# Kernel tuning notes

Hardware: AMD Instinct MI355X
Metric: run time of the kernel (lower is better)

Reference implementation:

```python
import jax, jax.numpy as jnp
import numpy as np

K = 3          # kernel size
STRIDE = 1
PAD = 1
DIL = 1
K2 = K * K


def setup_inputs() -> dict:
    key = jax.random.key(0)
    ks = jax.random.split(key, 5)
    B, Cin, Cout, H, W = 8, 128, 128, 64, 64
    x = jax.random.normal(ks[0], (B, Cin, H, W), jnp.float32)
    # conv_offset_mask: Conv2d(Cin, 3*dg*K*K=27, 3x3). Original inits to zero;
    # use small random weights so offsets are nonzero sub-pixel shifts.
    w_off = jax.random.normal(ks[1], (3 * K2, Cin, K, K), jnp.float32) * 0.05
    b_off = jax.random.normal(ks[2], (3 * K2,), jnp.float32) * 0.1
    weight = jax.random.normal(ks[3], (Cout, Cin, K, K), jnp.float32) / np.sqrt(Cin * K2)
    bias = jax.random.normal(ks[4], (Cout,), jnp.float32) * 0.1
    return dict(x=x, w_off=w_off, b_off=b_off, weight=weight, bias=bias)


def _conv(x, w, b):
    y = jax.lax.conv_general_dilated(
        x, w, (STRIDE, STRIDE), [(PAD, PAD), (PAD, PAD)],
        dimension_numbers=('NCHW', 'OIHW', 'NCHW'))
    return y + b[None, :, None, None]


def _sample_one(xb, pyb, pxb, mb):
    Cin, Hin, Win = xb.shape
    y0 = jnp.floor(pyb)
    x0 = jnp.floor(pxb)
    wy = pyb - y0   # fractional weights
    wx = pxb - x0
    y0i = y0.astype(jnp.int32)
    x0i = x0.astype(jnp.int32)
    xf = xb.reshape(Cin, -1)

    def g(yi, xi):
        valid = ((yi >= 0) & (yi < Hin) & (xi >= 0) & (xi < Win)).astype(xb.dtype)
        idx = jnp.clip(yi, 0, Hin - 1) * Win + jnp.clip(xi, 0, Win - 1)
        return xf[:, idx] * valid[None]   # [Cin,K2,Ho,Wo]

    v = (g(y0i, x0i) * ((1 - wy) * (1 - wx))[None]
         + g(y0i, x0i + 1) * ((1 - wy) * wx)[None]
         + g(y0i + 1, x0i) * (wy * (1 - wx))[None]
         + g(y0i + 1, x0i + 1) * (wy * wx)[None])
    return v * mb[None]   # modulated columns [Cin,K2,Ho,Wo]


def reference(x, w_off, b_off, weight, bias):
    B, Cin, Hin, Win = x.shape
    Cout = weight.shape[0]
    om = _conv(x, w_off, b_off)                 # [B, 3*K2, Ho, Wo]
    dy = om[:, :K2]
    dx = om[:, K2:2 * K2]
    m = jax.nn.sigmoid(om[:, 2 * K2:])          # modulation mask
    Ho, Wo = dy.shape[2], dy.shape[3]
    kh = jnp.repeat(jnp.arange(K), K)           # [K2] kernel row per tap
    kw = jnp.tile(jnp.arange(K), K)             # [K2] kernel col per tap
    grid_y = jnp.arange(Ho) * STRIDE - PAD
    grid_x = jnp.arange(Wo) * STRIDE - PAD
    py = dy + grid_y[None, None, :, None] + (kh * DIL)[None, :, None, None]
    px = dx + grid_x[None, None, None, :] + (kw * DIL)[None, :, None, None]
    cols = jax.vmap(_sample_one)(x, py, px, m)  # [B,Cin,K2,Ho,Wo]
    out = jnp.einsum('bckhw,ock->bohw', cols, weight.reshape(Cout, Cin, K2))
    return out + bias[None, :, None, None]
```

## Files before the change

### kernel.cpp

```cpp
#include <hip/hip_runtime.h>
#include <math.h>

#define BATCH 8
#define CIN   128
#define COUT  128
#define HH    64
#define WW    64
#define OC    27
#define KDIM  1152

typedef unsigned short u16;
typedef unsigned int   u32;
typedef __attribute__((ext_vector_type(8))) short bf16x8;
typedef __attribute__((ext_vector_type(4))) float f32x4;

__device__ __forceinline__ float b2f(u16 u) {
    return __uint_as_float((u32)u << 16);
}
__device__ __forceinline__ u16 f2b(float f) {
    u32 u = __float_as_uint(f);
    return (u16)((u + 0x7fffu + ((u >> 16) & 1u)) >> 16);
}
__device__ __forceinline__ float blo(u32 u) { return __uint_as_float(u << 16); }
__device__ __forceinline__ float bhi(u32 u) { return __uint_as_float(u & 0xffff0000u); }
__device__ __forceinline__ u32 cvtpk(float lo, float hi) {
    u32 r;
    asm("v_cvt_pk_bf16_f32 %0, %1, %2" : "=v"(r) : "v"(lo), "v"(hi));
    return r;
}
__device__ __forceinline__ bf16x8 pack8(u32 a, u32 b, u32 c, u32 d) {
    union { u32 u[4]; bf16x8 v; } z;
    z.u[0] = a; z.u[1] = b; z.u[2] = c; z.u[3] = d;
    return z.v;
}

__device__ __forceinline__ int xswiz(int o, int K) { return (o & 7) * K + (o >> 3); }

__global__ __launch_bounds__(256) void k_prep(const float* __restrict__ x,
                                              const float* __restrict__ weight,
                                              const float* __restrict__ w_off,
                                              u16* __restrict__ xtb,
                                              u16* __restrict__ wbf,
                                              u16* __restrict__ wop) {
    __shared__ float tile[64][65];
    int gbid = blockIdx.x;
    int t = threadIdx.x;
    if (gbid < 1024) {
        int bid = xswiz(gbid, 128);
        int b   = bid >> 7;
        int c0  = ((bid >> 6) & 1) << 6;
        int hw0 = (bid & 63) << 6;
        int ln  = t & 63;
        int cq  = t >> 6;
#pragma unroll
        for (int r = 0; r < 16; ++r) {
            int c_l = cq * 16 + r;
            tile[c_l][ln] = x[(((size_t)(b * CIN + c0 + c_l)) << 12) + hw0 + ln];
        }
        __syncthreads();
#pragma unroll
        for (int r = 0; r < 16; ++r) {
            int hw_w = cq * 16 + r;
            xtb[((size_t)(b << 12) + hw0 + hw_w) * 128 + c0 + ln] = f2b(tile[ln][hw_w]);
        }
    } else if (gbid < 1600) {
        int tid = (gbid - 1024) * 256 + t;
        int j  = tid & 7;
        int l  = (tid >> 3) & 63;
        int ni = (tid >> 9) & 7;
        int s  = (tid >> 12) & 3;
        int t9 = tid >> 14;
        int co = ni * 16 + (l & 15);
        int ci = s * 32 + ((l >> 4) << 3) + j;
        wbf[tid] = f2b(weight[co * KDIM + ci * 9 + t9]);
    } else {
        int tid = (gbid - 1600) * 256 + t;
        int j   = tid & 7;
        int l   = (tid >> 3) & 63;
        int ni  = (tid >> 9) & 1;
        int sg  = (tid >> 10) & 3;
        int rest = tid >> 12;
        int t9  = rest % 9;
        int split = rest / 9;
        int co = ni * 16 + (l & 15);
        int ci = sg * 32 + ((l >> 4) << 3) + j;
        float val = (co < OC) ? w_off[co * KDIM + ci * 9 + t9] : 0.f;
        u16 hi = f2b(val);
        u16 lo = f2b(val - b2f(hi));
        wop[tid] = split ? lo : hi;
    }
}

#define CST 228
__global__ __launch_bounds__(512, 4) void k_fused(const float* __restrict__ x,
                                                  const u16* __restrict__ xtb,
                                                  const u16* __restrict__ wop,
                                                  const u16* __restrict__ wbf,
                                                  const float* __restrict__ b_off,
                                                  const float* __restrict__ bias,
                                                  float* __restrict__ out) {
    __shared__ __align__(16) char smem[73472];
    float* Xf  = (float*)smem;
    float* red = (float*)(smem + 58368);
    float* omf = (float*)(smem + 66560);

    const int t  = threadIdx.x;
    const int lb = xswiz(blockIdx.x, 64);
    const int b  = lb >> 6;
    const int h  = lb & 63;
    const int l    = t & 63;
    const int wv   = t >> 6;
    const int l15  = l & 15;
    const int lg   = l >> 4;

    {
        const int ntile = wv & 3;
        const int kgrp  = wv >> 2;

        if (t < 192) {
            int ci = t & 63, row = t >> 6;
            int idx = ci * CST + row * 68 + (((ci >> 3) & 3) << 3) + 64;
            *(float4*)(Xf + idx) = make_float4(0.f, 0.f, 0.f, 0.f);
        }

        f32x4 acc0 = {0.f, 0.f, 0.f, 0.f};
        f32x4 acc1 = {0.f, 0.f, 0.f, 0.f};
        float4 st_[6];

        auto stageA_load = [&](int half) {
#pragma unroll
            for (int it = 0; it < 6; ++it) {
                int slot = t + it * 512;
                int pair = slot >> 4, ln16 = slot & 15;
                int row = pair >> 6, ci = pair & 63;
                int grow = h - 1 + row;
                float4 v = make_float4(0.f, 0.f, 0.f, 0.f);
                if ((unsigned)grow < 64u)
                    v = *(const float4*)(x + (((size_t)(b * CIN + half * 64 + ci)) << 12)
                                           + (grow << 6) + ln16 * 4);
                st_[it] = v;
            }
        };
        auto stageA_store = [&]() {
#pragma unroll
            for (int it = 0; it < 6; ++it) {
                int slot = t + it * 512;
                int pair = slot >> 4, ln16 = slot & 15;
                int row = pair >> 6, ci = pair & 63;
                int idx = ci * CST + row * 68 + (((ci >> 3) & 3) << 3) + ln16 * 4;
                *(float4*)(Xf + idx) = st_[it];
            }
        };
        auto kloopA = [&](int half) {
            for (int tap = 0; tap < 9; ++tap) {
                int kh = tap / 3, kw = tap - kh * 3;
                int gw = ntile * 16 + kw - 1 + l15;
                int px = (gw < 0) ? 64 : ((gw > 63) ? 65 : gw);
                int ci0 = kgrp * 32 + (lg << 3);
                int base = ci0 * CST + kh * 68 + (((ci0 >> 3) & 3) << 3) + px;
                float f0 = Xf[base], f1 = Xf[base + CST];
                float f2 = Xf[base + 2 * CST], f3 = Xf[base + 3 * CST];
                float f4 = Xf[base + 4 * CST], f5 = Xf[base + 5 * CST];
                float f6 = Xf[base + 6 * CST], f7 = Xf[base + 7 * CST];
                u32 h0 = cvtpk(f0, f1), h1 = cvtpk(f2, f3);
                u32 h2 = cvtpk(f4, f5), h3 = cvtpk(f6, f7);
                u32 l0 = cvtpk(f0 - blo(h0), f1 - bhi(h0));
                u32 l1 = cvtpk(f2 - blo(h1), f3 - bhi(h1));
                u32 l2 = cvtpk(f4 - blo(h2), f5 - bhi(h2));
                u32 l3 = cvtpk(f6 - blo(h3), f7 - bhi(h3));
                bf16x8 ah = pack8(h0, h1, h2, h3);
                bf16x8 al = pack8(l0, l1, l2, l3);
                int sg = half * 2 + kgrp;
                const u16* B = wop + (((tap * 4 + sg) * 2) << 9) + (l << 3);
                bf16x8 wh0 = *(const bf16x8*)(B);
                bf16x8 wh1 = *(const bf16x8*)(B + 512);
                bf16x8 wl0 = *(const bf16x8*)(B + 36864);
                bf16x8 wl1 = *(const bf16x8*)(B + 36864 + 512);
                acc0 = __builtin_amdgcn_mfma_f32_16x16x32_bf16(wh0, ah, acc0, 0, 0, 0);
                acc1 = __builtin_amdgcn_mfma_f32_16x16x32_bf16(wh1, ah, acc1, 0, 0, 0);
                acc0 = __builtin_amdgcn_mfma_f32_16x16x32_bf16(wl0, ah, acc0, 0, 0, 0);
                acc1 = __builtin_amdgcn_mfma_f32_16x16x32_bf16(wl1, ah, acc1, 0, 0, 0);
                acc0 = __builtin_amdgcn_mfma_f32_16x16x32_bf16(wh0, al, acc0, 0, 0, 0);
                acc1 = __builtin_amdgcn_mfma_f32_16x16x32_bf16(wh1, al, acc1, 0, 0, 0);
            }
        };

        stageA_load(0);
        stageA_store();
        __syncthreads();
        stageA_load(1);
        kloopA(0);
        __syncthreads();
        stageA_store();
        __syncthreads();
        kloopA(1);

        if (kgrp) {
            float* rp = red + (((ntile << 6) + l) << 3);
            *(f32x4*)rp = acc0;
            *(f32x4*)(rp + 4) = acc1;
        }
        __syncthreads();
        if (!kgrp) {
            const float* rp = red + (((ntile << 6) + l) << 3);
            acc0 += *(const f32x4*)rp;
            acc1 += *(const f32x4*)(rp + 4);
            int px = ntile * 16 + l15;
            int co0 = lg << 2;
#pragma unroll
            for (int r = 0; r < 4; ++r)
                omf[((co0 + r) << 6) + px] = acc0[r] + b_off[co0 + r];
            int co1 = 16 + (lg << 2);
#pragma unroll
            for (int r = 0; r < 4; ++r) {
                int co = co1 + r;
                if (co < OC) {
                    float v = acc1[r] + b_off[co];
                    if (co >= 18) v = 1.f / (1.f + expf(-v));
                    omf[(co << 6) + px] = v;
                }
            }
        }
        __syncthreads();
    }

    float (*w4)[4] = (float (*)[4])(smem + 32768);
    int* y0c = (int*)(smem + 41984);
    int* x0c = (int*)(smem + 44288);
    int* y1c = (int*)(smem + 46592);
    int* x1c = (int*)(smem + 48896);

    for (int i = t; i < 576; i += 512) {
        int p  = i / 9;
        int tt = i - p * 9;
        float dy = omf[(tt << 6) + p];
        float dx = omf[((9 + tt) << 6) + p];
        float m  = omf[((18 + tt) << 6) + p];
        float py = dy + (float)(h - 1 + tt / 3);
        float px = dx + (float)(p - 1 + tt % 3);
        float y0f = floorf(py), x0f = floorf(px);
        float wy = py - y0f, wx = px - x0f;
        int y0 = (int)y0f, x0 = (int)x0f;
        int y1 = y0 + 1,   x1 = x0 + 1;
        float vy0 = ((unsigned)y0 < 64u) ? 1.f : 0.f;
        float vy1 = ((unsigned)y1 < 64u) ? 1.f : 0.f;
        float vx0 = ((unsigned)x0 < 64u) ? 1.f : 0.f;
        float vx1 = ((unsigned)x1 < 64u) ? 1.f : 0.f;
        w4[i][0] = (1.f - wy) * (1.f - wx) * m * vy0 * vx0;
        w4[i][1] = (1.f - wy) * wx         * m * vy0 * vx1;
        w4[i][2] = wy         * (1.f - wx) * m * vy1 * vx0;
        w4[i][3] = wy         * wx         * m * vy1 * vx1;
        y0c[i] = min(max(y0, 0), 63);
        y1c[i] = min(max(y1, 0), 63);
        x0c[i] = min(max(x0, 0), 63);
        x1c[i] = min(max(x1, 0), 63);
    }
    __syncthreads();

    f32x4 acc[4][2];
#pragma unroll
    for (int pt = 0; pt < 4; ++pt)
#pragma unroll
        for (int nt = 0; nt < 2; ++nt) acc[pt][nt] = (f32x4){0.f, 0.f, 0.f, 0.f};

    const int grp  = t >> 8;
    const int tl   = t & 255;
    const int l2   = tl & 63;
    const int wv2  = tl >> 6;
    const int row0 = l2 & 15;
    const int kg   = l2 >> 4;

    const int sp = tl >> 2;
    const int sc = tl & 3;
    const u16* xb = xtb + ((size_t)b << 19);

    uint4 g_[2][4];

    auto sample_load = [&](int tt) {
        int pi = sp * 9 + tt;
        int o00 = (((y0c[pi] << 6) | x0c[pi]) << 7) + grp * 64;
        int o01 = (((y0c[pi] << 6) | x1c[pi]) << 7) + grp * 64;
        int o10 = (((y1c[pi] << 6) | x0c[pi]) << 7) + grp * 64;
        int o11 = (((y1c[pi] << 6) | x1c[pi]) << 7) + grp * 64;
#pragma unroll
        for (int k = 0; k < 2; ++k) {
            int ch = k * 32 + sc * 8;
            g_[k][0] = *(const uint4*)(xb + o00 + ch);
            g_[k][1] = *(const uint4*)(xb + o01 + ch);
            g_[k][2] = *(const uint4*)(xb + o10 + ch);
            g_[k][3] = *(const uint4*)(xb + o11 + ch);
        }
    };

    auto sample_finish = [&](int tt, int buf) {
        int pi = sp * 9 + tt;
        float4 W = *(const float4*)(&w4[pi][0]);
        u16* dst = (u16*)(smem + buf * 16384);
#pragma unroll
        for (int k = 0; k < 2; ++k) {
            uint4 a00 = g_[k][0], a01 = g_[k][1], a10 = g_[k][2], a11 = g_[k][3];
            uint4 ow;
            {
                float e0 = W.x * blo(a00.x) + W.y * blo(a01.x) + W.z * blo(a10.x) + W.w * blo(a11.x);
                float e1 = W.x * bhi(a00.x) + W.y * bhi(a01.x) + W.z * bhi(a10.x) + W.w * bhi(a11.x);
                ow.x = cvtpk(e0, e1);
            }
            {
                float e0 = W.x * blo(a00.y) + W.y * blo(a01.y) + W.z * blo(a10.y) + W.w * blo(a11.y);
                float e1 = W.x * bhi(a00.y) + W.y * bhi(a01.y) + W.z * bhi(a10.y) + W.w * bhi(a11.y);
                ow.y = cvtpk(e0, e1);
            }
            {
                float e0 = W.x * blo(a00.z) + W.y * blo(a01.z) + W.z * blo(a10.z) + W.w * blo(a11.z);
                float e1 = W.x * bhi(a00.z) + W.y * bhi(a01.z) + W.z * bhi(a10.z) + W.w * bhi(a11.z);
                ow.z = cvtpk(e0, e1);
            }
            {
                float e0 = W.x * blo(a00.w) + W.y * blo(a01.w) + W.z * blo(a10.w) + W.w * blo(a11.w);
                float e1 = W.x * bhi(a00.w) + W.y * bhi(a01.w) + W.z * bhi(a10.w) + W.w * bhi(a11.w);
                ow.w = cvtpk(e0, e1);
            }
            int q16 = (grp * 8 + k * 4 + sc) ^ (sp & 15);
            *(uint4*)((char*)dst + (sp << 8) + (q16 << 4)) = ow;
        }
    };

    auto domfma = [&](int t9, int buf) {
        const char* Ab = (const char*)(smem + buf * 16384);
#pragma unroll
        for (int shalf = 0; shalf < 2; ++shalf) {
            int s = grp * 2 + shalf;
            int q = s * 4 + kg;
            int sw = (q ^ row0) << 4;
            bf16x8 a[4];
#pragma unroll
            for (int pt = 0; pt < 4; ++pt)
                a[pt] = *(const bf16x8*)(Ab + ((pt * 16 + row0) << 8) + sw);
            const u16* B = wbf + ((size_t)t9 << 14) + (s << 12) + (wv2 << 10) + (l2 << 3);
            bf16x8 b0 = *(const bf16x8*)(B);
            bf16x8 b1 = *(const bf16x8*)(B + 512);
#pragma unroll
            for (int pt = 0; pt < 4; ++pt) {
                acc[pt][0] = __builtin_amdgcn_mfma_f32_16x16x32_bf16(a[pt], b0, acc[pt][0], 0, 0, 0);
                acc[pt][1] = __builtin_amdgcn_mfma_f32_16x16x32_bf16(a[pt], b1, acc[pt][1], 0, 0, 0);
            }
        }
    };

    sample_load(0);
    sample_finish(0, 0);
    __syncthreads();
    for (int tt = 0; tt < 9; ++tt) {
        if (tt < 8) sample_load(tt + 1);
        domfma(tt, tt & 1);
        if (tt < 8) sample_finish(tt + 1, (tt + 1) & 1);
        __syncthreads();
    }

    float* outs = (float*)smem;
    if (grp) {
#pragma unroll
        for (int pt = 0; pt < 4; ++pt)
#pragma unroll
            for (int nt = 0; nt < 2; ++nt) {
                int co  = wv2 * 32 + nt * 16 + row0;
                int pxq = pt * 4 + kg;
                *(f32x4*)((char*)outs + (co << 8) + ((pxq ^ (co & 7)) << 4)) = acc[pt][nt];
            }
    }
    __syncthreads();
    if (!grp) {
#pragma unroll
        for (int pt = 0; pt < 4; ++pt)
#pragma unroll
            for (int nt = 0; nt < 2; ++nt) {
                int co  = wv2 * 32 + nt * 16 + row0;
                int pxq = pt * 4 + kg;
                char* ad = (char*)outs + (co << 8) + ((pxq ^ (co & 7)) << 4);
                f32x4 v = *(const f32x4*)ad;
                *(f32x4*)ad = v + acc[pt][nt];
            }
    }
    __syncthreads();
    {
        int co = t >> 2, qt = t & 3;
        float bb = bias[co];
        float* og = out + (((size_t)(b * COUT + co)) << 12) + (h << 6);
#pragma unroll
        for (int j = 0; j < 4; ++j) {
            int pxq = qt * 4 + j;
            f32x4 v = *(const f32x4*)((const char*)outs + (co << 8) + ((pxq ^ (co & 7)) << 4));
            float4 r = make_float4(v.x + bb, v.y + bb, v.z + bb, v.w + bb);
            *reinterpret_cast<float4*>(og + pxq * 4) = r;
        }
    }
}

extern "C" void kernel_launch(void* const* d_in, const int* in_sizes, int n_in,
                              void* d_out, int out_size, void* d_ws, size_t ws_size,
                              hipStream_t stream) {
    const float* x      = (const float*)d_in[0];
    const float* w_off  = (const float*)d_in[1];
    const float* b_off  = (const float*)d_in[2];
    const float* weight = (const float*)d_in[3];
    const float* bias   = (const float*)d_in[4];
    float* out = (float*)d_out;

    u16* xtb = (u16*)d_ws;
    u16* wbf = xtb + 4194304;
    u16* wop = wbf + 147456;

    k_prep<<<1888, 256, 0, stream>>>(x, weight, w_off, xtb, wbf, wop);
    k_fused<<<512, 512, 0, stream>>>(x, xtb, wop, wbf, b_off, bias, out);
}
```

Before: 48.35 us.

## Shrink LDS footprint via 4-round offset-conv staging and packed sample indices

The offset-conv phase now stages 32 input channels per round over four rounds instead of 64 channels over two halves. That shrinks the fp32 staging buffer, and the shared allocation drops from about 73KB to about 52KB. Launch bounds rise from 4 to 6 waves per SIMD so more blocks can be resident. The four clamped bilinear corner indices are packed into one u32 per sample, and addresses are built from two base pointers plus a column delta. The trade-off is more barriers in the staging loop, half the waves idling each round, and tighter register limits from the higher launch bound.

```diff
diff --git a/kernel.cpp b/kernel.cpp
--- a/kernel.cpp
+++ b/kernel.cpp
@@ -8,6 +8,7 @@
 #define WW    64
 #define OC    27
 #define KDIM  1152
+#define CST   228
 
 typedef unsigned short u16;
 typedef unsigned int   u32;
@@ -91,18 +92,17 @@
     }
 }
 
-#define CST 228
-__global__ __launch_bounds__(512, 4) void k_fused(const float* __restrict__ x,
+__global__ __launch_bounds__(512, 6) void k_fused(const float* __restrict__ x,
                                                   const u16* __restrict__ xtb,
                                                   const u16* __restrict__ wop,
                                                   const u16* __restrict__ wbf,
                                                   const float* __restrict__ b_off,
                                                   const float* __restrict__ bias,
                                                   float* __restrict__ out) {
-    __shared__ __align__(16) char smem[73472];
+    __shared__ __align__(16) char smem[51632];
     float* Xf  = (float*)smem;
-    float* red = (float*)(smem + 58368);
-    float* omf = (float*)(smem + 66560);
+    float* red = (float*)(smem + 32768);
+    float* omf = (float*)(smem + 44288);
 
     const int t  = threadIdx.x;
     const int lb = xswiz(blockIdx.x, 64);
@@ -117,47 +117,47 @@
         const int ntile = wv & 3;
         const int kgrp  = wv >> 2;
 
-        if (t < 192) {
-            int ci = t & 63, row = t >> 6;
+        if (t < 96) {
+            int ci = t & 31, row = t >> 5;
             int idx = ci * CST + row * 68 + (((ci >> 3) & 3) << 3) + 64;
             *(float4*)(Xf + idx) = make_float4(0.f, 0.f, 0.f, 0.f);
         }
 
         f32x4 acc0 = {0.f, 0.f, 0.f, 0.f};
         f32x4 acc1 = {0.f, 0.f, 0.f, 0.f};
-        float4 st_[6];
-
-        auto stageA_load = [&](int half) {
-#pragma unroll
-            for (int it = 0; it < 6; ++it) {
+        float4 st_[3];
+
+        auto stageA_load = [&](int rnd) {
+#pragma unroll
+            for (int it = 0; it < 3; ++it) {
                 int slot = t + it * 512;
                 int pair = slot >> 4, ln16 = slot & 15;
-                int row = pair >> 6, ci = pair & 63;
+                int row = pair >> 5, ci = pair & 31;
                 int grow = h - 1 + row;
                 float4 v = make_float4(0.f, 0.f, 0.f, 0.f);
                 if ((unsigned)grow < 64u)
-                    v = *(const float4*)(x + (((size_t)(b * CIN + half * 64 + ci)) << 12)
+                    v = *(const float4*)(x + (((size_t)(b * CIN + rnd * 32 + ci)) << 12)
                                            + (grow << 6) + ln16 * 4);
                 st_[it] = v;
             }
         };
         auto stageA_store = [&]() {
 #pragma unroll
-            for (int it = 0; it < 6; ++it) {
+            for (int it = 0; it < 3; ++it) {
                 int slot = t + it * 512;
                 int pair = slot >> 4, ln16 = slot & 15;
-                int row = pair >> 6, ci = pair & 63;
+                int row = pair >> 5, ci = pair & 31;
                 int idx = ci * CST + row * 68 + (((ci >> 3) & 3) << 3) + ln16 * 4;
                 *(float4*)(Xf + idx) = st_[it];
             }
         };
-        auto kloopA = [&](int half) {
+        auto kloopA = [&](int rnd) {
             for (int tap = 0; tap < 9; ++tap) {
                 int kh = tap / 3, kw = tap - kh * 3;
                 int gw = ntile * 16 + kw - 1 + l15;
                 int px = (gw < 0) ? 64 : ((gw > 63) ? 65 : gw);
-                int ci0 = kgrp * 32 + (lg << 3);
-                int base = ci0 * CST + kh * 68 + (((ci0 >> 3) & 3) << 3) + px;
+                int ci0 = lg << 3;
+                int base = ci0 * CST + kh * 68 + (lg << 3) + px;
                 float f0 = Xf[base], f1 = Xf[base + CST];
                 float f2 = Xf[base + 2 * CST], f3 = Xf[base + 3 * CST];
                 float f4 = Xf[base + 4 * CST], f5 = Xf[base + 5 * CST];
@@ -170,8 +170,7 @@
                 u32 l3 = cvtpk(f6 - blo(h3), f7 - bhi(h3));
                 bf16x8 ah = pack8(h0, h1, h2, h3);
                 bf16x8 al = pack8(l0, l1, l2, l3);
-                int sg = half * 2 + kgrp;
-                const u16* B = wop + (((tap * 4 + sg) * 2) << 9) + (l << 3);
+                const u16* B = wop + (((tap * 4 + rnd) * 2) << 9) + (l << 3);
                 bf16x8 wh0 = *(const bf16x8*)(B);
                 bf16x8 wh1 = *(const bf16x8*)(B + 512);
                 bf16x8 wl0 = *(const bf16x8*)(B + 36864);
@@ -188,12 +187,12 @@
         stageA_load(0);
         stageA_store();
         __syncthreads();
-        stageA_load(1);
-        kloopA(0);
-        __syncthreads();
-        stageA_store();
-        __syncthreads();
-        kloopA(1);
+        for (int rnd = 0; rnd < 4; ++rnd) {
+            if (rnd < 3) stageA_load(rnd + 1);
+            if ((rnd >> 1) == kgrp) kloopA(rnd);
+            __syncthreads();
+            if (rnd < 3) { stageA_store(); __syncthreads(); }
+        }
 
         if (kgrp) {
             float* rp = red + (((ntile << 6) + l) << 3);
@@ -209,7 +208,7 @@
             int co0 = lg << 2;
 #pragma unroll
             for (int r = 0; r < 4; ++r)
-                omf[((co0 + r) << 6) + px] = acc0[r] + b_off[co0 + r];
+                omf[(co0 + r) * 68 + px] = acc0[r] + b_off[co0 + r];
             int co1 = 16 + (lg << 2);
 #pragma unroll
             for (int r = 0; r < 4; ++r) {
@@ -217,7 +216,7 @@
                 if (co < OC) {
                     float v = acc1[r] + b_off[co];
                     if (co >= 18) v = 1.f / (1.f + expf(-v));
-                    omf[(co << 6) + px] = v;
+                    omf[co * 68 + px] = v;
                 }
             }
         }
@@ -225,17 +224,14 @@
     }
 
     float (*w4)[4] = (float (*)[4])(smem + 32768);
-    int* y0c = (int*)(smem + 41984);
-    int* x0c = (int*)(smem + 44288);
-    int* y1c = (int*)(smem + 46592);
-    int* x1c = (int*)(smem + 48896);
+    u32* idxp = (u32*)(smem + 41984);
 
     for (int i = t; i < 576; i += 512) {
         int p  = i / 9;
         int tt = i - p * 9;
-        float dy = omf[(tt << 6) + p];
-        float dx = omf[((9 + tt) << 6) + p];
-        float m  = omf[((18 + tt) << 6) + p];
+        float dy = omf[tt * 68 + p];
+        float dx = omf[(9 + tt) * 68 + p];
+        float m  = omf[(18 + tt) * 68 + p];
         float py = dy + (float)(h - 1 + tt / 3);
         float px = dx + (float)(p - 1 + tt % 3);
         float y0f = floorf(py), x0f = floorf(px);
@@ -250,10 +246,11 @@
         w4[i][1] = (1.f - wy) * wx         * m * vy0 * vx1;
         w4[i][2] = wy         * (1.f - wx) * m * vy1 * vx0;
         w4[i][3] = wy         * wx         * m * vy1 * vx1;
-        y0c[i] = min(max(y0, 0), 63);
-        y1c[i] = min(max(y1, 0), 63);
-        x0c[i] = min(max(x0, 0), 63);
-        x1c[i] = min(max(x1, 0), 63);
+        int y0c = min(max(y0, 0), 63);
+        int y1c = min(max(y1, 0), 63);
+        int x0c = min(max(x0, 0), 63);
+        int x1c = min(max(x1, 0), 63);
+        idxp[i] = (u32)y0c | ((u32)y1c << 8) | ((u32)x0c << 16) | ((u32)x1c << 24);
     }
     __syncthreads();
 
@@ -277,19 +274,20 @@
     uint4 g_[2][4];
 
     auto sample_load = [&](int tt) {
-        int pi = sp * 9 + tt;
-        int o00 = (((y0c[pi] << 6) | x0c[pi]) << 7) + grp * 64;
-        int o01 = (((y0c[pi] << 6) | x1c[pi]) << 7) + grp * 64;
-        int o10 = (((y1c[pi] << 6) | x0c[pi]) << 7) + grp * 64;
-        int o11 = (((y1c[pi] << 6) | x1c[pi]) << 7) + grp * 64;
-#pragma unroll
-        for (int k = 0; k < 2; ++k) {
-            int ch = k * 32 + sc * 8;
-            g_[k][0] = *(const uint4*)(xb + o00 + ch);
-            g_[k][1] = *(const uint4*)(xb + o01 + ch);
-            g_[k][2] = *(const uint4*)(xb + o10 + ch);
-            g_[k][3] = *(const uint4*)(xb + o11 + ch);
-        }
+        u32 pk = idxp[sp * 9 + tt];
+        int y0 = pk & 255, y1 = (pk >> 8) & 255;
+        int x0 = (pk >> 16) & 255, x1 = pk >> 24;
+        int d1 = (x1 - x0) << 7;
+        const u16* p0 = xb + (((y0 << 6) | x0) << 7) + grp * 64 + sc * 8;
+        const u16* p1 = xb + (((y1 << 6) | x0) << 7) + grp * 64 + sc * 8;
+        g_[0][0] = *(const uint4*)(p0);
+        g_[0][1] = *(const uint4*)(p0 + d1);
+        g_[0][2] = *(const uint4*)(p1);
+        g_[0][3] = *(const uint4*)(p1 + d1);
+        g_[1][0] = *(const uint4*)(p0 + 32);
+        g_[1][1] = *(const uint4*)(p0 + d1 + 32);
+        g_[1][2] = *(const uint4*)(p1 + 32);
+        g_[1][3] = *(const uint4*)(p1 + d1 + 32);
     };
 
     auto sample_finish = [&](int tt, int buf) {
```

After: 123.8 us. 2.56x slower.
